# Kernel optimization log

Measured on AMD Instinct MI355X. Metric: run time of the kernel, lower is better.

## Reference

```python
import jax, jax.numpy as jnp
import numpy as np

N = 50000      # nodes
E = 800000     # edges (avg degree 16)
DIM = 256      # in_channels == heads * out_channels
H = 8          # heads
C = DIM // H   # per-head out_channels = 32
EDGE_DIM = 2
NEG_SLOPE = 0.2


def setup_inputs() -> dict:
    key = jax.random.key(0)
    ks = jax.random.split(key, 8)
    x = jax.random.normal(ks[0], (N, DIM), dtype=jnp.float32)
    edge_index = jax.random.randint(ks[1], (2, E), 0, N, dtype=jnp.int32)
    edge_attr = jax.random.normal(ks[2], (E, EDGE_DIM), dtype=jnp.float32)
    s = 1.0 / np.sqrt(DIM)
    W_l = jax.random.normal(ks[3], (DIM, H * C), dtype=jnp.float32) * s   # lin_l (src)
    W_r = jax.random.normal(ks[4], (DIM, H * C), dtype=jnp.float32) * s   # lin_r (dst)
    W_e = jax.random.normal(ks[5], (EDGE_DIM, H * C), dtype=jnp.float32) * (1.0 / np.sqrt(EDGE_DIM))
    att = jax.random.normal(ks[6], (H, C), dtype=jnp.float32) * s         # attention vector a
    bias = jnp.zeros((H * C,), dtype=jnp.float32)
    return {"x": x, "edge_index": edge_index, "edge_attr": edge_attr,
            "W_l": W_l, "W_r": W_r, "W_e": W_e, "att": att, "bias": bias}


def reference(x, edge_index, edge_attr, W_l, W_r, W_e, att, bias):
    src, dst = edge_index[0], edge_index[1]
    # --- add self loops; fill_value='mean' => scatter-mean of incoming edge_attr per node ---
    attr_sum = jax.ops.segment_sum(edge_attr, dst, num_segments=N)          # [N, 2]
    cnt = jax.ops.segment_sum(jnp.ones((edge_attr.shape[0], 1), edge_attr.dtype), dst, num_segments=N)
    loop_attr = attr_sum / jnp.maximum(cnt, 1.0)                             # [N, 2], 0 for isolated nodes
    idx = jnp.arange(N, dtype=src.dtype)
    src_a = jnp.concatenate([src, idx])                                      # [E+N]
    dst_a = jnp.concatenate([dst, idx])
    ea = jnp.concatenate([edge_attr, loop_attr], axis=0)                     # [E+N, 2]
    # --- GATv2: project src/dst/edge features ---
    x_l = (x @ W_l).reshape(N, H, C)
    x_r = (x @ W_r).reshape(N, H, C)
    e_e = (ea @ W_e).reshape(-1, H, C)                                       # [E+N, H, C]
    m = x_l[src_a] + x_r[dst_a] + e_e                                        # [E+N, H, C]
    score = jnp.einsum('ehc,hc->eh', jax.nn.leaky_relu(m, NEG_SLOPE), att)   # [E+N, H]
    # --- segment softmax over incoming edges of each dst (self loop guarantees >=1 edge) ---
    smax = jax.ops.segment_max(score, dst_a, num_segments=N)                 # [N, H]
    ex = jnp.exp(score - smax[dst_a])
    denom = jax.ops.segment_sum(ex, dst_a, num_segments=N)                   # [N, H]
    alpha = ex / denom[dst_a]                                                # [E+N, H]
    # --- weighted scatter-add of src messages ---
    out = jax.ops.segment_sum(alpha[..., None] * x_l[src_a], dst_a, num_segments=N)  # [N, H, C]
    return out.reshape(N, H * C) + bias
```

## Files before the change

kernel.cpp:

```cpp
#include <hip/hip_runtime.h>
#include <hip/hip_bf16.h>

#define NN 50000
#define EE 800000
#define DIM 256
#define ROWC 64
#define NEG_SLOPE 0.2f
#define LOG2E 1.44269504088896f

#define GEMM_BLOCKS 1564
#define CF_BLOCKS   3125
#define ZERO_BLOCKS 49
#define WT_BLOCKS   512

typedef __attribute__((ext_vector_type(8))) short short8;
typedef __attribute__((ext_vector_type(4))) float f32x4;
typedef __attribute__((ext_vector_type(2))) float v2f;

__device__ __forceinline__ unsigned short f2bf(float f) {
    unsigned u = __float_as_uint(f);
    unsigned r = (u + 0x7fffu + ((u >> 16) & 1u)) >> 16;
    return (unsigned short)r;
}
__device__ __forceinline__ float u2f_lo(unsigned u) {
    return __uint_as_float(u << 16);
}
__device__ __forceinline__ float u2f_hi(unsigned u) {
    return __uint_as_float(u & 0xffff0000u);
}

__device__ __forceinline__ float red8(float s) {
    int t;
    t = __builtin_amdgcn_update_dpp(0, __float_as_int(s), 0xB1, 0xF, 0xF, true);
    s += __int_as_float(t);
    t = __builtin_amdgcn_update_dpp(0, __float_as_int(s), 0x4E, 0xF, 0xF, true);
    s += __int_as_float(t);
    t = __builtin_amdgcn_update_dpp(0, __float_as_int(s), 0x141, 0xF, 0xF, true);
    s += __int_as_float(t);
    return s;
}

__global__ __launch_bounds__(256) void k_prep0(
    const float* __restrict__ Wl, const float* __restrict__ Wr,
    unsigned short* __restrict__ wt, int* __restrict__ cnt)
{
    int b = blockIdx.x;
    if (b < ZERO_BLOCKS) {
        *(int4*)(cnt + (b * 256 + threadIdx.x) * 4) = make_int4(0, 0, 0, 0);
    } else {
        int idx = (b - ZERO_BLOCKS) * 256 + threadIdx.x;
        int n = idx >> 8, k = idx & 255;
        float v = (n < 256) ? Wl[k * 256 + n] : Wr[k * 256 + (n - 256)];
        wt[idx] = f2bf(v);
    }
}

__global__ __launch_bounds__(256) void k_main(
    const float* __restrict__ x, const unsigned short* __restrict__ wt,
    const int* __restrict__ ei, const float* __restrict__ ea,
    int* __restrict__ cnt, unsigned short* __restrict__ xl,
    unsigned short* __restrict__ xr, uint2* __restrict__ edge_rec)
{
    __shared__ short sAB[12288];
    int tid = threadIdx.x;

    if (blockIdx.x >= GEMM_BLOCKS) {
        int e = (blockIdx.x - GEMM_BLOCKS) * 256 + tid;
        int src = ei[e];
        int dst = ei[EE + e];
        float2 a = *(const float2*)(ea + 2 * e);
        int rl = atomicAdd(cnt + dst, 1);
        if (rl < ROWC) {
            unsigned packed = ((unsigned)f2bf(a.y) << 16) | f2bf(a.x);
            edge_rec[(size_t)dst * ROWC + rl] = make_uint2((unsigned)src, packed);
        }
        return;
    }

    int bid = blockIdx.x;
    const int q = GEMM_BLOCKS / 8, r = GEMM_BLOCKS % 8;
    int xcd = bid & 7, kk = bid >> 3;
    int wg = (xcd < r) ? xcd * (q + 1) + kk
                       : r * (q + 1) + (xcd - r) * q + kk;

    int wid = tid >> 6, lane = tid & 63;
    int mt = wg >> 2, nt = wg & 3;
    int mBase = mt * 128, nBase = nt * 128;
    int wm = (wid & 1) * 64, wn = (wid >> 1) * 64;
    int qq4 = lane >> 4, mh = lane & 15;

    f32x4 acc[4][4];
#pragma unroll
    for (int i = 0; i < 4; ++i)
#pragma unroll
        for (int j = 0; j < 4; ++j)
            acc[i][j] = (f32x4){0.f, 0.f, 0.f, 0.f};

    int aoffF[4], boff[4];
#pragma unroll
    for (int f = 0; f < 4; ++f) {
        int rr = wm + f * 16 + mh;
        aoffF[f] = rr * 32 + ((qq4 ^ (rr & 3)) << 3);
        int nl = wn + f * 16 + mh;
        boff[f] = 8192 + (nl * 4 + (qq4 ^ (nl & 3))) * 8;
    }

    for (int k0 = 0; k0 < 256; k0 += 32) {
        __syncthreads();
#pragma unroll
        for (int it = 0; it < 6; ++it) {
            int L = it * 256 + tid;
            const void* g;
            if (L < 1024) {
                int rr = L >> 3;
                int qs = (L >> 1) & 3, hf = L & 1;
                int q2 = qs ^ (rr & 3);
                int grow = mBase + rr;
                if (grow > NN - 1) grow = NN - 1;
                g = (const void*)(x + (size_t)grow * 256 + k0 + q2 * 8 + hf * 4);
            } else {
                int LB = L - 1024;
                int nl = LB >> 2;
                int q2 = (LB & 3) ^ (nl & 3);
                g = (const void*)(wt + (size_t)(nBase + nl) * 256 + k0 + q2 * 8);
            }
            short* lp = sAB + (it * 256 + wid * 64) * 8;
            __builtin_amdgcn_global_load_lds(
                (const __attribute__((address_space(1))) void*)g,
                (__attribute__((address_space(3))) void*)lp, 16, 0, 0);
        }
        __syncthreads();

        short8 af[4], bfr[4];
        const float* sAf = (const float*)sAB;
#pragma unroll
        for (int f = 0; f < 4; ++f) {
            f32x4 lo = *(const f32x4*)(sAf + aoffF[f]);
            f32x4 hi = *(const f32x4*)(sAf + aoffF[f] + 4);
            uint4 up;
            asm("v_cvt_pk_bf16_f32 %0, %1, %2" : "=v"(up.x) : "v"(lo[0]), "v"(lo[1]));
            asm("v_cvt_pk_bf16_f32 %0, %1, %2" : "=v"(up.y) : "v"(lo[2]), "v"(lo[3]));
            asm("v_cvt_pk_bf16_f32 %0, %1, %2" : "=v"(up.z) : "v"(hi[0]), "v"(hi[1]));
            asm("v_cvt_pk_bf16_f32 %0, %1, %2" : "=v"(up.w) : "v"(hi[2]), "v"(hi[3]));
            af[f] = *(short8*)&up;
        }
#pragma unroll
        for (int f = 0; f < 4; ++f) bfr[f] = *(const short8*)(sAB + boff[f]);
#pragma unroll
        for (int i = 0; i < 4; ++i)
#pragma unroll
            for (int j = 0; j < 4; ++j)
                acc[i][j] = __builtin_amdgcn_mfma_f32_16x16x32_bf16(
                    af[i], bfr[j], acc[i][j], 0, 0, 0);
    }

    unsigned short* cb = (nt < 2) ? xl : xr;
    int chalf = (nt & 1) * 128;
#pragma unroll
    for (int i = 0; i < 4; ++i)
#pragma unroll
        for (int j = 0; j < 4; ++j)
#pragma unroll
            for (int rr = 0; rr < 4; ++rr) {
                int row = mBase + wm + i * 16 + qq4 * 4 + rr;
                if (row < NN) {
                    int col = chalf + wn + j * 16 + mh;
                    cb[(size_t)row * 256 + col] = f2bf(acc[i][j][rr]);
                }
            }
}

__global__ __launch_bounds__(256) void k_attn(
    const unsigned short* __restrict__ xl, const unsigned short* __restrict__ xr,
    const int* __restrict__ cnt, const uint2* __restrict__ edge_rec,
    const float* __restrict__ W_e, const float* __restrict__ att,
    const float* __restrict__ bias, float* __restrict__ out)
{
    int n = __builtin_amdgcn_readfirstlane(blockIdx.x * 4 + (threadIdx.x >> 6));
    if (n >= NN) return;
    int lane = threadIdx.x & 63;
    int j = lane * 4;

    uint2 xru = *(const uint2*)(xr + ((size_t)n << 8) + j);
    v2f xr01 = {u2f_lo(xru.x), u2f_hi(xru.x)};
    v2f xr23 = {u2f_lo(xru.y), u2f_hi(xru.y)};
    float4 av = *(const float4*)(att + j);
    v2f att01 = {av.x * LOG2E, av.y * LOG2E};
    v2f att23 = {av.z * LOG2E, av.w * LOG2E};
    float4 w0v = *(const float4*)(W_e + j);
    float4 w1v = *(const float4*)(W_e + 256 + j);
    v2f we0_01 = {w0v.x, w0v.y}, we0_23 = {w0v.z, w0v.w};
    v2f we1_01 = {w1v.x, w1v.y}, we1_23 = {w1v.z, w1v.w};
    const v2f sl2 = {NEG_SLOPE, NEG_SLOPE};

    int cn = __builtin_amdgcn_readfirstlane(cnt[n]);
    if (cn > ROWC) cn = ROWC;
    int rs = n << 6;

    float D = 0.0f, la0 = 0.0f, la1 = 0.0f;
    v2f acc01 = {0.f, 0.f}, acc23 = {0.f, 0.f};

    auto body = [&](uint2 ru, float a0, float a1) {
        v2f xl01 = {u2f_lo(ru.x), u2f_hi(ru.x)};
        v2f xl23 = {u2f_lo(ru.y), u2f_hi(ru.y)};
        v2f a0v = {a0, a0}, a1v = {a1, a1};
        v2f m01 = xl01 + xr01;
        v2f m23 = xl23 + xr23;
        m01 = __builtin_elementwise_fma(a0v, we0_01, m01);
        m23 = __builtin_elementwise_fma(a0v, we0_23, m23);
        m01 = __builtin_elementwise_fma(a1v, we1_01, m01);
        m23 = __builtin_elementwise_fma(a1v, we1_23, m23);
        v2f t01 = __builtin_elementwise_max(m01, m01 * sl2);
        v2f t23 = __builtin_elementwise_max(m23, m23 * sl2);
        v2f sv = t01 * att01;
        sv = __builtin_elementwise_fma(t23, att23, sv);
        float s = sv.x + sv.y;
        s = red8(s);
        float w = __builtin_amdgcn_exp2f(s);
        D += w;
        v2f wv = {w, w};
        acc01 = __builtin_elementwise_fma(wv, xl01, acc01);
        acc23 = __builtin_elementwise_fma(wv, xl23, acc23);
    };

    if (cn > 0) {
        uint2 rc = edge_rec[rs + lane];
        int rcx = (int)rc.x, rca = (int)rc.y;

        auto gat = [&](int k) -> uint2 {
            unsigned sidx = (unsigned)__builtin_amdgcn_readlane(rcx, k);
            if (sidx > NN - 1) sidx = 0;
            return *(const uint2*)(xl + ((size_t)sidx << 8) + j);
        };
        auto proc = [&](uint2 xu, int k) {
            unsigned pk = (unsigned)__builtin_amdgcn_readlane(rca, k);
            float a0 = __uint_as_float(pk << 16);
            float a1 = __uint_as_float(pk & 0xffff0000u);
            la0 += a0; la1 += a1;
            body(xu, a0, a1);
        };

        int m = cn;
        uint2 x0 = gat(0), x1 = gat(1), x2 = gat(2), x3 = gat(3);
        uint2 x4 = gat(4), x5 = gat(5), x6 = gat(6), x7 = gat(7);
        for (int i = 0; i < m; i += 8) {
            proc(x0, i);
            if (i +  8 < m) x0 = gat(i +  8);
            if (i + 1 < m) { proc(x1, i + 1); if (i +  9 < m) x1 = gat(i +  9); }
            if (i + 2 < m) { proc(x2, i + 2); if (i + 10 < m) x2 = gat(i + 10); }
            if (i + 3 < m) { proc(x3, i + 3); if (i + 11 < m) x3 = gat(i + 11); }
            if (i + 4 < m) { proc(x4, i + 4); if (i + 12 < m) x4 = gat(i + 12); }
            if (i + 5 < m) { proc(x5, i + 5); if (i + 13 < m) x5 = gat(i + 13); }
            if (i + 6 < m) { proc(x6, i + 6); if (i + 14 < m) x6 = gat(i + 14); }
            if (i + 7 < m) { proc(x7, i + 7); if (i + 15 < m) x7 = gat(i + 15); }
        }
    }

    float invc = 1.0f / fmaxf((float)cn, 1.0f);
    uint2 xs = *(const uint2*)(xl + ((size_t)n << 8) + j);
    body(xs, la0 * invc, la1 * invc);

    float invD = 1.0f / D;
    float4 b4 = *(const float4*)(bias + j);
    float4 o;
    o.x = fmaf(acc01.x, invD, b4.x);
    o.y = fmaf(acc01.y, invD, b4.y);
    o.z = fmaf(acc23.x, invD, b4.z);
    o.w = fmaf(acc23.y, invD, b4.w);
    *(float4*)(out + (size_t)n * 256 + j) = o;
}

extern "C" void kernel_launch(void* const* d_in, const int* in_sizes, int n_in,
                              void* d_out, int out_size, void* d_ws, size_t ws_size,
                              hipStream_t stream)
{
    const float* x    = (const float*)d_in[0];
    const int*   ei   = (const int*)  d_in[1];
    const float* ea   = (const float*)d_in[2];
    const float* Wl   = (const float*)d_in[3];
    const float* Wr   = (const float*)d_in[4];
    const float* We   = (const float*)d_in[5];
    const float* att  = (const float*)d_in[6];
    const float* bias = (const float*)d_in[7];
    float* out = (float*)d_out;

    char* ws = (char*)d_ws;
    size_t off = 0;
    unsigned short* xl = (unsigned short*)(ws + off); off += (size_t)NN * 256 * 2;
    unsigned short* xr = (unsigned short*)(ws + off); off += (size_t)NN * 256 * 2;
    uint2*  edge_rec   = (uint2*)(ws + off);          off += (size_t)(NN * ROWC + 128) * 8;
    int*    cnt        = (int*)(ws + off);            off += (size_t)(ZERO_BLOCKS * 1024) * 4;
    unsigned short* wt = (unsigned short*)(ws + off); off += (size_t)512 * 256 * 2;

    k_prep0 <<<ZERO_BLOCKS + WT_BLOCKS, 256, 0, stream>>>(Wl, Wr, wt, cnt);
    k_main  <<<GEMM_BLOCKS + CF_BLOCKS, 256, 0, stream>>>(
        x, wt, ei, ea, cnt, xl, xr, edge_rec);
    k_attn  <<<12500, 256, 0, stream>>>(
        xl, xr, cnt, edge_rec, We, att, bias, out);
}
```

Before: 242.8 us.

## Load GEMM fragments directly from global memory, dropping LDS staging

The projection GEMM no longer stages A (x) and B (packed weights) tiles through shared memory with global_load_lds and barriers. Each lane now reads its MFMA fragments straight from global memory through per-lane pointers, and the k loop is fully unrolled. This removes the LDS footprint and the __syncthreads, which may raise occupancy and let loads run ahead. In exchange, warps that share rows or columns read the same data redundantly through the caches, and the per-lane accesses are less coalesced.

```diff
diff --git a/kernel.cpp b/kernel.cpp
--- a/kernel.cpp
+++ b/kernel.cpp
@@ -8,8 +8,8 @@
 #define NEG_SLOPE 0.2f
 #define LOG2E 1.44269504088896f
 
+#define CF_BLOCKS   3125
 #define GEMM_BLOCKS 1564
-#define CF_BLOCKS   3125
 #define ZERO_BLOCKS 49
 #define WT_BLOCKS   512
 
@@ -61,7 +61,6 @@
     int* __restrict__ cnt, unsigned short* __restrict__ xl,
     unsigned short* __restrict__ xr, uint2* __restrict__ edge_rec)
 {
-    __shared__ short sAB[12288];
     int tid = threadIdx.x;
 
     if (blockIdx.x >= GEMM_BLOCKS) {
@@ -78,16 +77,26 @@
     }
 
     int bid = blockIdx.x;
-    const int q = GEMM_BLOCKS / 8, r = GEMM_BLOCKS % 8;
+    const int qc = GEMM_BLOCKS / 8, rc = GEMM_BLOCKS % 8;
     int xcd = bid & 7, kk = bid >> 3;
-    int wg = (xcd < r) ? xcd * (q + 1) + kk
-                       : r * (q + 1) + (xcd - r) * q + kk;
+    int wg = (xcd < rc) ? xcd * (qc + 1) + kk
+                        : rc * (qc + 1) + (xcd - rc) * qc + kk;
 
     int wid = tid >> 6, lane = tid & 63;
     int mt = wg >> 2, nt = wg & 3;
     int mBase = mt * 128, nBase = nt * 128;
     int wm = (wid & 1) * 64, wn = (wid >> 1) * 64;
-    int qq4 = lane >> 4, mh = lane & 15;
+    int q = lane >> 4, mh = lane & 15;
+
+    const float* pa[4];
+    const unsigned short* pb[4];
+#pragma unroll
+    for (int f = 0; f < 4; ++f) {
+        int ra = mBase + wm + f * 16 + mh;
+        if (ra > NN - 1) ra = NN - 1;
+        pa[f] = x + (size_t)ra * 256 + q * 8;
+        pb[f] = wt + (size_t)(nBase + wn + f * 16 + mh) * 256 + q * 8;
+    }
 
     f32x4 acc[4][4];
 #pragma unroll
@@ -96,56 +105,21 @@
         for (int j = 0; j < 4; ++j)
             acc[i][j] = (f32x4){0.f, 0.f, 0.f, 0.f};
 
-    int aoffF[4], boff[4];
-#pragma unroll
-    for (int f = 0; f < 4; ++f) {
-        int rr = wm + f * 16 + mh;
-        aoffF[f] = rr * 32 + ((qq4 ^ (rr & 3)) << 3);
-        int nl = wn + f * 16 + mh;
-        boff[f] = 8192 + (nl * 4 + (qq4 ^ (nl & 3))) * 8;
-    }
-
+#pragma unroll
     for (int k0 = 0; k0 < 256; k0 += 32) {
-        __syncthreads();
-#pragma unroll
-        for (int it = 0; it < 6; ++it) {
-            int L = it * 256 + tid;
-            const void* g;
-            if (L < 1024) {
-                int rr = L >> 3;
-                int qs = (L >> 1) & 3, hf = L & 1;
-                int q2 = qs ^ (rr & 3);
-                int grow = mBase + rr;
-                if (grow > NN - 1) grow = NN - 1;
-                g = (const void*)(x + (size_t)grow * 256 + k0 + q2 * 8 + hf * 4);
-            } else {
-                int LB = L - 1024;
-                int nl = LB >> 2;
-                int q2 = (LB & 3) ^ (nl & 3);
-                g = (const void*)(wt + (size_t)(nBase + nl) * 256 + k0 + q2 * 8);
-            }
-            short* lp = sAB + (it * 256 + wid * 64) * 8;
-            __builtin_amdgcn_global_load_lds(
-                (const __attribute__((address_space(1))) void*)g,
-                (__attribute__((address_space(3))) void*)lp, 16, 0, 0);
-        }
-        __syncthreads();
-
         short8 af[4], bfr[4];
-        const float* sAf = (const float*)sAB;
 #pragma unroll
         for (int f = 0; f < 4; ++f) {
-            f32x4 lo = *(const f32x4*)(sAf + aoffF[f]);
-            f32x4 hi = *(const f32x4*)(sAf + aoffF[f] + 4);
+            f32x4 lo = *(const f32x4*)(pa[f] + k0);
+            f32x4 hi = *(const f32x4*)(pa[f] + k0 + 4);
             uint4 up;
             asm("v_cvt_pk_bf16_f32 %0, %1, %2" : "=v"(up.x) : "v"(lo[0]), "v"(lo[1]));
             asm("v_cvt_pk_bf16_f32 %0, %1, %2" : "=v"(up.y) : "v"(lo[2]), "v"(lo[3]));
             asm("v_cvt_pk_bf16_f32 %0, %1, %2" : "=v"(up.z) : "v"(hi[0]), "v"(hi[1]));
             asm("v_cvt_pk_bf16_f32 %0, %1, %2" : "=v"(up.w) : "v"(hi[2]), "v"(hi[3]));
             af[f] = *(short8*)&up;
+            bfr[f] = *(const short8*)(pb[f] + k0);
         }
-#pragma unroll
-        for (int f = 0; f < 4; ++f) bfr[f] = *(const short8*)(sAB + boff[f]);
 #pragma unroll
         for (int i = 0; i < 4; ++i)
 #pragma unroll
@@ -162,7 +136,7 @@
         for (int j = 0; j < 4; ++j)
 #pragma unroll
             for (int rr = 0; rr < 4; ++rr) {
-                int row = mBase + wm + i * 16 + qq4 * 4 + rr;
+                int row = mBase + wm + i * 16 + q * 4 + rr;
                 if (row < NN) {
                     int col = chalf + wn + j * 16 + mh;
                     cb[(size_t)row * 256 + col] = f2bf(acc[i][j][rr]);
```

Result: slower. 289.2 us (+19.1%).
